# Optimization experiments

Measured on AMD Instinct MI355X. Metric: run time of the kernel, lower is better.

## Reference

```python
import jax, jax.numpy as jnp
import numpy as np

N_EDGES = 800_000
N_NODES = 50_000
D_MODEL = 128
D_IN = 2 * D_MODEL  # received-edge aggregate concat node features


def setup_inputs() -> dict:
    key = jax.random.key(0)
    k_e, k_n, k_r, k_w = jax.random.split(key, 4)
    edges = jax.random.normal(k_e, (N_EDGES, D_MODEL), dtype=jnp.float32)
    nodes = jax.random.normal(k_n, (N_NODES, D_MODEL), dtype=jnp.float32)
    receivers = jax.random.randint(k_r, (N_EDGES,), 0, N_NODES, dtype=jnp.int64)
    # nn.Linear(d_in, d_model, bias=False); stored as [d_in, d_model] so y = x @ W
    W = jax.random.normal(k_w, (D_IN, D_MODEL), dtype=jnp.float32) * (1.0 / np.sqrt(D_IN))
    return {"edges": edges, "nodes": nodes, "receivers": receivers, "W": W}


def reference(edges, nodes, receivers, W):
    n_nodes = nodes.shape[0]
    # unsorted_mean_agg: scatter-add edges into receiver nodes, divide by counts
    seg_sum = jax.ops.segment_sum(edges, receivers, num_segments=n_nodes)  # [N, D]
    counts = jax.ops.segment_sum(
        jnp.ones((edges.shape[0],), dtype=edges.dtype), receivers, num_segments=n_nodes
    )
    agg = seg_sum / jnp.maximum(counts, 1.0)[:, None]  # segment mean
    collected = jnp.concatenate([agg, nodes], axis=-1)  # [N, 2*D]
    updated_nodes = collected @ W  # project; update_fn = identity
    return updated_nodes
```

## Files before the change

### kernel.cpp

```cpp
#include <hip/hip_runtime.h>
#include <hip/hip_bf16.h>

#define N_EDGES  800000
#define N_NODES  50000
#define D_MODEL  128
#define D_IN     256
#define NBLK_SCAN 196

typedef __attribute__((ext_vector_type(8))) short short8;
typedef __attribute__((ext_vector_type(4))) float f32x4;

static __device__ __forceinline__ unsigned short f2bf(float f) {
    unsigned int u = __builtin_bit_cast(unsigned int, f);
    u += 0x7FFFu + ((u >> 16) & 1u);
    return (unsigned short)(u >> 16);
}

__global__ __launch_bounds__(256) void init_kernel(
    int* __restrict__ cnt, const float* __restrict__ W,
    unsigned short* __restrict__ Wt)
{
    int g = blockIdx.x * 256 + threadIdx.x;
    if (g < N_NODES) cnt[g] = 0;
    if (g < D_IN * D_MODEL) {
        int k = g >> 7;
        int c = g & 127;
        Wt[c * 256 + k] = f2bf(W[g]);
    }
}

__global__ __launch_bounds__(256) void hist_kernel(
    const int* __restrict__ recv, int* __restrict__ cnt)
{
    int stride = gridDim.x * blockDim.x;
    for (int e = blockIdx.x * blockDim.x + threadIdx.x; e < N_EDGES; e += stride)
        atomicAdd(&cnt[recv[e]], 1);
}

__global__ __launch_bounds__(256) void scan_partial_kernel(
    const int* __restrict__ cnt, int* __restrict__ partial)
{
    __shared__ int s[256];
    int t = threadIdx.x;
    int i = blockIdx.x * 256 + t;
    s[t] = (i < N_NODES) ? cnt[i] : 0;
    __syncthreads();
    for (int off = 128; off > 0; off >>= 1) {
        if (t < off) s[t] += s[t + off];
        __syncthreads();
    }
    if (t == 0) partial[blockIdx.x] = s[0];
}

__global__ __launch_bounds__(256) void scan_root_kernel(
    const int* __restrict__ partial, int* __restrict__ root)
{
    __shared__ int s[256];
    int t = threadIdx.x;
    s[t] = (t < NBLK_SCAN) ? partial[t] : 0;
    __syncthreads();
    for (int off = 1; off < 256; off <<= 1) {
        int tmp = (t >= off) ? s[t - off] : 0;
        __syncthreads();
        s[t] += tmp;
        __syncthreads();
    }
    if (t < NBLK_SCAN) root[t] = (t == 0) ? 0 : s[t - 1];
}

__global__ __launch_bounds__(256) void scan_expand_kernel(
    const int* __restrict__ cnt, const int* __restrict__ root,
    int* __restrict__ offs, int* __restrict__ cursor)
{
    __shared__ int s[256];
    int t = threadIdx.x;
    int i = blockIdx.x * 256 + t;
    int v = (i < N_NODES) ? cnt[i] : 0;
    s[t] = v;
    __syncthreads();
    for (int off = 1; off < 256; off <<= 1) {
        int tmp = (t >= off) ? s[t - off] : 0;
        __syncthreads();
        s[t] += tmp;
        __syncthreads();
    }
    int excl = root[blockIdx.x] + s[t] - v;
    if (i < N_NODES) { offs[i] = excl; cursor[i] = excl; }
    if (blockIdx.x == 0 && t == 0) offs[N_NODES] = N_EDGES;
}

__global__ __launch_bounds__(256) void scatter_idx_kernel(
    const int* __restrict__ recv, int* __restrict__ cursor, int* __restrict__ eidx)
{
    int stride = gridDim.x * blockDim.x;
    for (int e = blockIdx.x * blockDim.x + threadIdx.x; e < N_EDGES; e += stride) {
        int pos = atomicAdd(&cursor[recv[e]], 1);
        eidx[pos] = e;
    }
}

#define LDK 264

__global__ __launch_bounds__(256) void fused_agg_gemm_kernel(
    const float4*         __restrict__ edges4,
    const int*            __restrict__ offs,
    const int*            __restrict__ eidx,
    const float*          __restrict__ nodes,
    const unsigned short* __restrict__ Wt,
    float*                __restrict__ out)
{
    __shared__ unsigned short As[64][LDK];

    const int t = threadIdx.x;
    const int rowBase = blockIdx.x * 64;
    const int wv   = t >> 6;
    const int lane = t & 63;
    const int sub  = lane >> 5;
    const int col4 = lane & 31;

    #pragma unroll
    for (int it = 0; it < 4; ++it) {
        int chunk = it * 256 + t;
        int r  = chunk >> 4;
        int c8 = (chunk & 15) * 8;
        int gr = rowBase + r;
        float4 v0 = make_float4(0.f, 0.f, 0.f, 0.f);
        float4 v1 = make_float4(0.f, 0.f, 0.f, 0.f);
        if (gr < N_NODES) {
            const float* p = nodes + (size_t)gr * 128 + c8;
            v0 = *(const float4*)p;
            v1 = *(const float4*)(p + 4);
        }
        short8 s;
        s[0] = (short)f2bf(v0.x); s[1] = (short)f2bf(v0.y);
        s[2] = (short)f2bf(v0.z); s[3] = (short)f2bf(v0.w);
        s[4] = (short)f2bf(v1.x); s[5] = (short)f2bf(v1.y);
        s[6] = (short)f2bf(v1.z); s[7] = (short)f2bf(v1.w);
        *(short8*)&As[r][128 + c8] = s;
    }

    int oidx = rowBase + wv * 16 + (lane < 16 ? lane : 16);
    if (oidx > N_NODES) oidx = N_NODES;
    int off_l = offs[oidx];

    for (int i = 0; i < 16; ++i) {
        int r   = wv * 16 + i;
        int beg = __shfl(off_l, i, 64);
        int end = __shfl(off_l, i + 1, 64);

        float ax = 0.f, ay = 0.f, az = 0.f, aw = 0.f;

        for (int base = beg; base < end; base += 64) {
            int m = end - base; if (m > 64) m = 64;
            int ei = 0;
            if (lane < m) ei = eidx[base + lane];

            int e = 0;
            for (; e + 16 <= m; e += 16) {
                int   idx[8];
                float4 v[8];
                #pragma unroll
                for (int j = 0; j < 8; ++j)
                    idx[j] = __shfl(ei, e + 2 * j + sub, 64);
                #pragma unroll
                for (int j = 0; j < 8; ++j)
                    v[j] = edges4[(size_t)idx[j] * 32 + col4];
                #pragma unroll
                for (int j = 0; j < 8; ++j) {
                    ax += v[j].x; ay += v[j].y; az += v[j].z; aw += v[j].w;
                }
            }
            for (; e + 8 <= m; e += 8) {
                int i0 = __shfl(ei, e + 0 + sub, 64);
                int i1 = __shfl(ei, e + 2 + sub, 64);
                int i2 = __shfl(ei, e + 4 + sub, 64);
                int i3 = __shfl(ei, e + 6 + sub, 64);
                float4 v0 = edges4[(size_t)i0 * 32 + col4];
                float4 v1 = edges4[(size_t)i1 * 32 + col4];
                float4 v2 = edges4[(size_t)i2 * 32 + col4];
                float4 v3 = edges4[(size_t)i3 * 32 + col4];
                ax += v0.x + v1.x + v2.x + v3.x;
                ay += v0.y + v1.y + v2.y + v3.y;
                az += v0.z + v1.z + v2.z + v3.z;
                aw += v0.w + v1.w + v2.w + v3.w;
            }
            for (; e + 2 <= m; e += 2) {
                int i0 = __shfl(ei, e + sub, 64);
                float4 v = edges4[(size_t)i0 * 32 + col4];
                ax += v.x; ay += v.y; az += v.z; aw += v.w;
            }
            if (e < m) {
                int i0 = __shfl(ei, e, 64);
                if (sub == 0) {
                    float4 v = edges4[(size_t)i0 * 32 + col4];
                    ax += v.x; ay += v.y; az += v.z; aw += v.w;
                }
            }
        }

        ax += __shfl_xor(ax, 32, 64);
        ay += __shfl_xor(ay, 32, 64);
        az += __shfl_xor(az, 32, 64);
        aw += __shfl_xor(aw, 32, 64);

        if (sub == 0) {
            float inv = 1.0f / fmaxf((float)(end - beg), 1.0f);
            ushort4 w;
            w.x = f2bf(ax * inv); w.y = f2bf(ay * inv);
            w.z = f2bf(az * inv); w.w = f2bf(aw * inv);
            *(ushort4*)&As[r][col4 * 4] = w;
        }
    }
    __syncthreads();

    const int lr = lane & 15;
    const int kb = lane >> 4;

    short8 a[8];
    #pragma unroll
    for (int ks = 0; ks < 8; ++ks)
        a[ks] = *(const short8*)&As[wv * 16 + lr][ks * 32 + kb * 8];

    #pragma unroll
    for (int cp = 0; cp < 4; ++cp) {
        int ct0 = cp * 2, ct1 = cp * 2 + 1;
        short8 b0[8], b1[8];
        #pragma unroll
        for (int ks = 0; ks < 8; ++ks) {
            b0[ks] = *(const short8*)(Wt + (size_t)(ct0 * 16 + lr) * 256 + ks * 32 + kb * 8);
            b1[ks] = *(const short8*)(Wt + (size_t)(ct1 * 16 + lr) * 256 + ks * 32 + kb * 8);
        }
        f32x4 acc0 = {0.f, 0.f, 0.f, 0.f};
        f32x4 acc1 = {0.f, 0.f, 0.f, 0.f};
        #pragma unroll
        for (int ks = 0; ks < 8; ++ks) {
            acc0 = __builtin_amdgcn_mfma_f32_16x16x32_bf16(a[ks], b0[ks], acc0, 0, 0, 0);
            acc1 = __builtin_amdgcn_mfma_f32_16x16x32_bf16(a[ks], b1[ks], acc1, 0, 0, 0);
        }
        #pragma unroll
        for (int r = 0; r < 4; ++r) {
            int gr = rowBase + wv * 16 + kb * 4 + r;
            if (gr < N_NODES) {
                out[(size_t)gr * 128 + ct0 * 16 + lr] = acc0[r];
                out[(size_t)gr * 128 + ct1 * 16 + lr] = acc1[r];
            }
        }
    }
}

extern "C" void kernel_launch(void* const* d_in, const int* in_sizes, int n_in,
                              void* d_out, int out_size, void* d_ws, size_t ws_size,
                              hipStream_t stream) {
    const float* edges = (const float*)d_in[0];
    const float* nodes = (const float*)d_in[1];
    const int*   recv  = (const int*)d_in[2];
    const float* W     = (const float*)d_in[3];
    float* out = (float*)d_out;

    char* base = (char*)d_ws;
    size_t o = 0;
    auto alloc = [&](size_t bytes) {
        size_t r = o; o = (o + bytes + 255) & ~(size_t)255; return r;
    };
    int*            cnt     = (int*)(base + alloc(N_NODES * 4));
    int*            offs    = (int*)(base + alloc((N_NODES + 1) * 4));
    int*            cursor  = (int*)(base + alloc(N_NODES * 4));
    int*            eidx    = (int*)(base + alloc(N_EDGES * 4));
    int*            partial = (int*)(base + alloc(NBLK_SCAN * 4));
    int*            root    = (int*)(base + alloc(NBLK_SCAN * 4));
    unsigned short* Wt      = (unsigned short*)(base + alloc(D_IN * D_MODEL * 2));

    init_kernel<<<dim3(NBLK_SCAN), dim3(256), 0, stream>>>(cnt, W, Wt);
    hist_kernel<<<dim3(2048), dim3(256), 0, stream>>>(recv, cnt);
    scan_partial_kernel<<<dim3(NBLK_SCAN), dim3(256), 0, stream>>>(cnt, partial);
    scan_root_kernel<<<dim3(1), dim3(256), 0, stream>>>(partial, root);
    scan_expand_kernel<<<dim3(NBLK_SCAN), dim3(256), 0, stream>>>(cnt, root, offs, cursor);
    scatter_idx_kernel<<<dim3(2048), dim3(256), 0, stream>>>(recv, cursor, eidx);

    fused_agg_gemm_kernel<<<dim3((N_NODES + 63) / 64), dim3(256), 0, stream>>>(
        (const float4*)edges, offs, eidx, nodes, Wt, out);
}
```

Measured before the change: 214.7 us.

## Gather edges as float2 per lane and fold root scan into expand

```diff
diff --git a/kernel.cpp b/kernel.cpp
--- a/kernel.cpp
+++ b/kernel.cpp
@@ -52,39 +52,28 @@
     if (t == 0) partial[blockIdx.x] = s[0];
 }
 
-__global__ __launch_bounds__(256) void scan_root_kernel(
-    const int* __restrict__ partial, int* __restrict__ root)
-{
+__global__ __launch_bounds__(256) void scan_expand_kernel(
+    const int* __restrict__ cnt, const int* __restrict__ partial,
+    int* __restrict__ offs, int* __restrict__ cursor)
+{
+    __shared__ int sp[256];
     __shared__ int s[256];
     int t = threadIdx.x;
-    s[t] = (t < NBLK_SCAN) ? partial[t] : 0;
-    __syncthreads();
-    for (int off = 1; off < 256; off <<= 1) {
-        int tmp = (t >= off) ? s[t - off] : 0;
-        __syncthreads();
-        s[t] += tmp;
-        __syncthreads();
-    }
-    if (t < NBLK_SCAN) root[t] = (t == 0) ? 0 : s[t - 1];
-}
-
-__global__ __launch_bounds__(256) void scan_expand_kernel(
-    const int* __restrict__ cnt, const int* __restrict__ root,
-    int* __restrict__ offs, int* __restrict__ cursor)
-{
-    __shared__ int s[256];
-    int t = threadIdx.x;
+
+    sp[t] = (t < NBLK_SCAN) ? partial[t] : 0;
     int i = blockIdx.x * 256 + t;
     int v = (i < N_NODES) ? cnt[i] : 0;
     s[t] = v;
     __syncthreads();
     for (int off = 1; off < 256; off <<= 1) {
-        int tmp = (t >= off) ? s[t - off] : 0;
+        int tp = (t >= off) ? sp[t - off] : 0;
+        int ts = (t >= off) ? s[t - off] : 0;
         __syncthreads();
-        s[t] += tmp;
+        sp[t] += tp; s[t] += ts;
         __syncthreads();
     }
-    int excl = root[blockIdx.x] + s[t] - v;
+    int base = (blockIdx.x == 0) ? 0 : sp[blockIdx.x - 1];
+    int excl = base + s[t] - v;
     if (i < N_NODES) { offs[i] = excl; cursor[i] = excl; }
     if (blockIdx.x == 0 && t == 0) offs[N_NODES] = N_EDGES;
 }
@@ -102,7 +91,7 @@
 #define LDK 264
 
 __global__ __launch_bounds__(256) void fused_agg_gemm_kernel(
-    const float4*         __restrict__ edges4,
+    const float2*         __restrict__ edges2,
     const int*            __restrict__ offs,
     const int*            __restrict__ eidx,
     const float*          __restrict__ nodes,
@@ -115,8 +104,6 @@
     const int rowBase = blockIdx.x * 64;
     const int wv   = t >> 6;
     const int lane = t & 63;
-    const int sub  = lane >> 5;
-    const int col4 = lane & 31;
 
     #pragma unroll
     for (int it = 0; it < 4; ++it) {
@@ -139,77 +126,49 @@
         *(short8*)&As[r][128 + c8] = s;
     }
 
-    int oidx = rowBase + wv * 16 + (lane < 16 ? lane : 16);
-    if (oidx > N_NODES) oidx = N_NODES;
-    int off_l = offs[oidx];
-
     for (int i = 0; i < 16; ++i) {
-        int r   = wv * 16 + i;
-        int beg = __shfl(off_l, i, 64);
-        int end = __shfl(off_l, i + 1, 64);
-
-        float ax = 0.f, ay = 0.f, az = 0.f, aw = 0.f;
-
-        for (int base = beg; base < end; base += 64) {
-            int m = end - base; if (m > 64) m = 64;
-            int ei = 0;
-            if (lane < m) ei = eidx[base + lane];
-
-            int e = 0;
-            for (; e + 16 <= m; e += 16) {
-                int   idx[8];
-                float4 v[8];
-                #pragma unroll
-                for (int j = 0; j < 8; ++j)
-                    idx[j] = __shfl(ei, e + 2 * j + sub, 64);
-                #pragma unroll
-                for (int j = 0; j < 8; ++j)
-                    v[j] = edges4[(size_t)idx[j] * 32 + col4];
-                #pragma unroll
-                for (int j = 0; j < 8; ++j) {
-                    ax += v[j].x; ay += v[j].y; az += v[j].z; aw += v[j].w;
-                }
+        int r    = wv * 16 + i;
+        int node = rowBase + r;
+        int beg = 0, end = 0;
+        if (node < N_NODES) {
+            beg = offs[node];
+            end = offs[node + 1];
+        }
+
+        float ax = 0.f, ay = 0.f;
+
+        int e = beg;
+        for (; e + 16 <= end; e += 16) {
+            float2 v[16];
+            #pragma unroll
+            for (int j = 0; j < 16; ++j) {
+                int ii = eidx[e + j];
+                v[j] = edges2[(size_t)ii * 64 + lane];
             }
-            for (; e + 8 <= m; e += 8) {
-                int i0 = __shfl(ei, e + 0 + sub, 64);
-                int i1 = __shfl(ei, e + 2 + sub, 64);
-                int i2 = __shfl(ei, e + 4 + sub, 64);
-                int i3 = __shfl(ei, e + 6 + sub, 64);
-                float4 v0 = edges4[(size_t)i0 * 32 + col4];
-                float4 v1 = edges4[(size_t)i1 * 32 + col4];
-                float4 v2 = edges4[(size_t)i2 * 32 + col4];
-                float4 v3 = edges4[(size_t)i3 * 32 + col4];
-                ax += v0.x + v1.x + v2.x + v3.x;
-                ay += v0.y + v1.y + v2.y + v3.y;
-                az += v0.z + v1.z + v2.z + v3.z;
-                aw += v0.w + v1.w + v2.w + v3.w;
+            #pragma unroll
+            for (int j = 0; j < 16; ++j) { ax += v[j].x; ay += v[j].y; }
+        }
+        for (; e + 4 <= end; e += 4) {
+            float2 v[4];
+            #pragma unroll
+            for (int j = 0; j < 4; ++j) {
+                int ii = eidx[e + j];
+                v[j] = edges2[(size_t)ii * 64 + lane];
             }
-            for (; e + 2 <= m; e += 2) {
-                int i0 = __shfl(ei, e + sub, 64);
-                float4 v = edges4[(size_t)i0 * 32 + col4];
-                ax += v.x; ay += v.y; az += v.z; aw += v.w;
-            }
-            if (e < m) {
-                int i0 = __shfl(ei, e, 64);
-                if (sub == 0) {
-                    float4 v = edges4[(size_t)i0 * 32 + col4];
-                    ax += v.x; ay += v.y; az += v.z; aw += v.w;
-                }
-            }
-        }
-
-        ax += __shfl_xor(ax, 32, 64);
-        ay += __shfl_xor(ay, 32, 64);
-        az += __shfl_xor(az, 32, 64);
-        aw += __shfl_xor(aw, 32, 64);
-
-        if (sub == 0) {
-            float inv = 1.0f / fmaxf((float)(end - beg), 1.0f);
-            ushort4 w;
-            w.x = f2bf(ax * inv); w.y = f2bf(ay * inv);
-            w.z = f2bf(az * inv); w.w = f2bf(aw * inv);
-            *(ushort4*)&As[r][col4 * 4] = w;
-        }
+            #pragma unroll
+            for (int j = 0; j < 4; ++j) { ax += v[j].x; ay += v[j].y; }
+        }
+        for (; e < end; ++e) {
+            int ii = eidx[e];
+            float2 v = edges2[(size_t)ii * 64 + lane];
+            ax += v.x; ay += v.y;
+        }
+
+        float inv = 1.0f / fmaxf((float)(end - beg), 1.0f);
+        ushort2 w;
+        w.x = f2bf(ax * inv);
+        w.y = f2bf(ay * inv);
+        *(ushort2*)&As[r][lane * 2] = w;
     }
     __syncthreads();
 
@@ -267,16 +226,14 @@
     int*            cursor  = (int*)(base + alloc(N_NODES * 4));
     int*            eidx    = (int*)(base + alloc(N_EDGES * 4));
     int*            partial = (int*)(base + alloc(NBLK_SCAN * 4));
-    int*            root    = (int*)(base + alloc(NBLK_SCAN * 4));
     unsigned short* Wt      = (unsigned short*)(base + alloc(D_IN * D_MODEL * 2));
 
     init_kernel<<<dim3(NBLK_SCAN), dim3(256), 0, stream>>>(cnt, W, Wt);
     hist_kernel<<<dim3(2048), dim3(256), 0, stream>>>(recv, cnt);
     scan_partial_kernel<<<dim3(NBLK_SCAN), dim3(256), 0, stream>>>(cnt, partial);
-    scan_root_kernel<<<dim3(1), dim3(256), 0, stream>>>(partial, root);
-    scan_expand_kernel<<<dim3(NBLK_SCAN), dim3(256), 0, stream>>>(cnt, root, offs, cursor);
+    scan_expand_kernel<<<dim3(NBLK_SCAN), dim3(256), 0, stream>>>(cnt, partial, offs, cursor);
     scatter_idx_kernel<<<dim3(2048), dim3(256), 0, stream>>>(recv, cursor, eidx);
 
     fused_agg_gemm_kernel<<<dim3((N_NODES + 63) / 64), dim3(256), 0, stream>>>(
-        (const float4*)edges, offs, eidx, nodes, Wt, out);
-}
+        (const float2*)edges, offs, eidx, nodes, Wt, out);
+}
```

After: 230.8 us. +7.5%, slower.
